# Kernel optimization log

Measured on AMD Instinct MI355X. Metric: run time of the kernel, lower is better.

## Reference

```python
import jax, jax.numpy as jnp
import numpy as np

N, E = 50000, 800000
IN_DIM, HID, HEADS, OUT = 128, 16, 8, 64
SLOPE = 0.2  # DGL GATConv default negative_slope


def setup_inputs() -> dict:
    key = jax.random.key(0)
    ks = jax.random.split(key, 12)
    return {
        "features": jax.random.normal(ks[0], (N, IN_DIM), jnp.float32),
        "src": jax.random.randint(ks[1], (E,), 0, N, jnp.int32),
        "dst": jax.random.randint(ks[2], (E,), 0, N, jnp.int32),
        "w": jax.random.uniform(ks[3], (E,), jnp.float32),
        "W1": jax.random.normal(ks[4], (IN_DIM, HEADS * HID), jnp.float32) / np.sqrt(IN_DIM),
        "al1": jax.random.normal(ks[5], (HEADS, HID), jnp.float32) * 0.1,
        "ar1": jax.random.normal(ks[6], (HEADS, HID), jnp.float32) * 0.1,
        "b1": jnp.zeros((HEADS * HID,), jnp.float32),
        "W2": jax.random.normal(ks[7], (HEADS * HID, OUT), jnp.float32) / np.sqrt(HEADS * HID),
        "al2": jax.random.normal(ks[8], (1, OUT), jnp.float32) * 0.1,
        "ar2": jax.random.normal(ks[9], (1, OUT), jnp.float32) * 0.1,
        "b2": jnp.zeros((OUT,), jnp.float32),
    }


def _gat_layer(x, src, dst, w, W, al, ar, b, heads, dout, act):
    """DGL GATConv with edge_weight: proj -> edge attn -> edge softmax(dst) -> * w -> scatter-sum."""
    n = x.shape[0]
    h = (x @ W).reshape(n, heads, dout)                 # [N,H,D]
    el = (h * al[None]).sum(-1)                         # [N,H] left attn logits
    er = (h * ar[None]).sum(-1)                         # [N,H] right attn logits
    e = el[src] + er[dst]                               # [E,H]
    e = jnp.where(e > 0, e, SLOPE * e)                  # leaky_relu
    m = jax.ops.segment_max(e, dst, num_segments=n)     # per-dst max for stable softmax
    a = jnp.exp(e - m[dst])
    z = jax.ops.segment_sum(a, dst, num_segments=n)
    a = (a / z[dst]) * w[:, None]                       # edge softmax scaled by edge weight
    msg = a[:, :, None] * h[src]                        # [E,H,D] gathered weighted messages
    rst = jax.ops.segment_sum(msg, dst, num_segments=n) # [N,H,D] scatter aggregation
    rst = rst + b.reshape(1, heads, dout)               # GATConv bias
    return act(rst) if act is not None else rst


def reference(features, src, dst, w, W1, al1, ar1, b1, W2, al2, ar2, b2):
    h = _gat_layer(features, src, dst, w, W1, al1, ar1, b1, HEADS, HID, jax.nn.relu)
    h = jax.nn.relu(h).reshape(N, HEADS * HID)          # outer F.relu + flatten(1)
    out = _gat_layer(h, src, dst, w, W2, al2, ar2, b2, 1, OUT, None)
    return out.squeeze(1)                               # [N,OUT]
```

## Files before the change

kernel.cpp:

```cpp
#include <hip/hip_runtime.h>
#include <hip/hip_fp16.h>

#define NN 50000
#define NE 800000

#define NBK 196
#define BSH 8
#define BMASK 255
#define SCAP 5120
#define CHUNK 1024
#define NBLK_A ((NE + CHUNK - 1) / CHUNK)

typedef _Float16 f16x8 __attribute__((ext_vector_type(8)));
typedef float f32x4 __attribute__((ext_vector_type(4)));


__global__ __launch_bounds__(256) void initg_k(int* gcur) {
    if (threadIdx.x < NBK) gcur[threadIdx.x] = 0;
}

__global__ __launch_bounds__(256) void sortA_k(const int* __restrict__ src,
                                               const int* __restrict__ dst,
                                               const float* __restrict__ wE,
                                               int* __restrict__ gcur,
                                               int2* __restrict__ stage) {
    __shared__ int hcnt[NBK], lexcl[NBK], lcur[NBK], gbase[NBK];
    __shared__ int wsum[4];
    __shared__ int2 lbuf[CHUNK];
    const int t = threadIdx.x;
    const int e0 = blockIdx.x * CHUNK;
    const int ne = min(CHUNK, NE - e0);
    if (t < NBK) { hcnt[t] = 0; lcur[t] = 0; }
    __syncthreads();
    for (int i = t; i < ne; i += 256) atomicAdd(&hcnt[dst[e0 + i] >> BSH], 1);
    __syncthreads();
    {
        const int lane = t & 63, wid = t >> 6;
        const int v = (t < NBK) ? hcnt[t] : 0;
        int s = v;
        #pragma unroll
        for (int off = 1; off < 64; off <<= 1) {
            int u = __shfl_up(s, off, 64);
            if (lane >= off) s += u;
        }
        if (lane == 63) wsum[wid] = s;
        __syncthreads();
        int add = 0;
        for (int w = 0; w < wid; w++) add += wsum[w];
        if (t < NBK) lexcl[t] = s - v + add;
    }
    __syncthreads();
    if (t < NBK && hcnt[t] > 0) gbase[t] = atomicAdd(&gcur[t], hcnt[t]);
    __syncthreads();
    for (int i = t; i < ne; i += 256) {
        const int d = dst[e0 + i];
        const int b = d >> BSH;
        const int r = atomicAdd(&lcur[b], 1);
        lbuf[lexcl[b] + r] = make_int2((src[e0 + i] & 0xFFFF) | ((d & BMASK) << 16),
                                       __float_as_int(wE[e0 + i]));
    }
    __syncthreads();
    const int wv = t >> 6, lane = t & 63;
    for (int b = wv; b < NBK; b += 4) {
        const int cnt = hcnt[b];
        if (cnt == 0) continue;
        const int lo = lexcl[b];
        int2* dp = stage + (size_t)b * SCAP + gbase[b];
        for (int j = lane; j < cnt; j += 64) dp[j] = lbuf[lo + j];
    }
}

__global__ __launch_bounds__(256) void scang_k(const int* __restrict__ gcur,
                                               int* __restrict__ gb2,
                                               int* __restrict__ offs_last) {
    __shared__ int wsum[4];
    const int t = threadIdx.x, lane = t & 63, wid = t >> 6;
    const int v = (t < NBK) ? gcur[t] : 0;
    int s = v;
    #pragma unroll
    for (int off = 1; off < 64; off <<= 1) {
        int u = __shfl_up(s, off, 64);
        if (lane >= off) s += u;
    }
    if (lane == 63) wsum[wid] = s;
    __syncthreads();
    int add = 0;
    for (int w = 0; w < wid; w++) add += wsum[w];
    if (t < NBK) gb2[t] = s - v + add;
    if (t == 0) offs_last[0] = NE;
}

__global__ __launch_bounds__(512) void sortB_k(const int* __restrict__ gcur,
                                               const int* __restrict__ gb2,
                                               const int2* __restrict__ stage,
                                               int* __restrict__ offs,
                                               unsigned int* __restrict__ csr) {
    __shared__ int cnt[256], cur[256];
    __shared__ int wsum[8];
    const int b = blockIdx.x, t = threadIdx.x;
    const int nb = gcur[b];
    const int base = gb2[b];
    const int dlo = b << BSH;
    if (t < 256) cnt[t] = 0;
    __syncthreads();
    const int2* sp = stage + (size_t)b * SCAP;
    for (int i = t; i < nb; i += 512) atomicAdd(&cnt[(sp[i].x >> 16) & BMASK], 1);
    __syncthreads();
    {
        const int lane = t & 63, wid = t >> 6;
        const int v = (t < 256) ? cnt[t] : 0;
        int s = v;
        #pragma unroll
        for (int off = 1; off < 64; off <<= 1) {
            int u = __shfl_up(s, off, 64);
            if (lane >= off) s += u;
        }
        if (lane == 63) wsum[wid] = s;
        __syncthreads();
        int add = 0;
        for (int w = 0; w < wid; w++) add += wsum[w];
        const int excl = s - v + add;
        if (t < 256) {
            cur[t] = excl;
            if (dlo + t < NN) offs[dlo + t] = base + excl;
        }
        if (t == 0) offs[min(dlo + 256, NN)] = base + nb;
    }
    __syncthreads();
    for (int i = t; i < nb; i += 512) {
        const int2 pr = sp[i];
        const int dloc = (pr.x >> 16) & BMASK;
        const int sv = pr.x & 0xFFFF;
        const int r = atomicAdd(&cur[dloc], 1);
        const __half hw = __float2half(__int_as_float(pr.y));
        csr[base + r] = (unsigned int)sv | ((unsigned int)__half_as_ushort(hw) << 16);
    }
}

__global__ __launch_bounds__(256) void convw_k(const float* __restrict__ W1,
                                               const float* __restrict__ W2,
                                               __half* __restrict__ w1t,
                                               __half* __restrict__ w2t) {
    int i = blockIdx.x * 256 + threadIdx.x;
    if (i < 128 * 128) {
        const int k = i >> 7, n = i & 127;
        w1t[(size_t)n * 128 + k] = __float2half(W1[i]);
    }
    if (i < 128 * 64) {
        const int k = i >> 6, n = i & 63;
        w2t[(size_t)n * 128 + k] = __float2half(W2[i]);
    }
}

__global__ __launch_bounds__(256) void proj1_k(const float* __restrict__ x,
                                               const __half* __restrict__ w1t,
                                               const float* __restrict__ al1,
                                               const float* __restrict__ ar1,
                                               __half* __restrict__ h1h,
                                               float* __restrict__ el1,
                                               float* __restrict__ er1) {
    const int t = threadIdx.x, l = t & 63, wv = t >> 6;
    const int rbase = blockIdx.x * 64 + wv * 16;
    const int cl = l & 15, kg = l >> 4;
    const int arow = rbase + cl;
    const float* xrow = x + (size_t)(arow < NN ? arow : NN - 1) * 128;
    f16x8 afrag[4];
    #pragma unroll
    for (int ks = 0; ks < 4; ks++) {
        const float4 u0 = *(const float4*)(xrow + ks * 32 + kg * 8);
        const float4 u1 = *(const float4*)(xrow + ks * 32 + kg * 8 + 4);
        f16x8 a;
        a[0] = (_Float16)u0.x; a[1] = (_Float16)u0.y; a[2] = (_Float16)u0.z; a[3] = (_Float16)u0.w;
        a[4] = (_Float16)u1.x; a[5] = (_Float16)u1.y; a[6] = (_Float16)u1.z; a[7] = (_Float16)u1.w;
        afrag[ks] = a;
    }
    f32x4 acc[8];
    #pragma unroll
    for (int nt = 0; nt < 8; nt++) { acc[nt][0]=0.f; acc[nt][1]=0.f; acc[nt][2]=0.f; acc[nt][3]=0.f; }
    #pragma unroll
    for (int nt = 0; nt < 8; nt++) {
        const f16x8* bp = (const f16x8*)(w1t + (size_t)(nt * 16 + cl) * 128 + kg * 8);
        #pragma unroll
        for (int ks = 0; ks < 4; ks++)
            acc[nt] = __builtin_amdgcn_mfma_f32_16x16x32_f16(afrag[ks], bp[ks * 4], acc[nt], 0, 0, 0);
    }
    const int orow0 = rbase + kg * 4;
    #pragma unroll
    for (int nt = 0; nt < 8; nt++) {
        const int col = nt * 16 + cl;
        const float alc = al1[col], arc = ar1[col];
        #pragma unroll
        for (int r = 0; r < 4; r++) {
            const float v = acc[nt][r];
            const int orow = orow0 + r;
            const bool ok = (orow < NN);
            if (ok) h1h[(size_t)orow * 128 + col] = __float2half(v);
            float pe = v * alc, pr = v * arc;
            #pragma unroll
            for (int m = 1; m < 16; m <<= 1) {
                pe += __shfl_xor(pe, m, 64);
                pr += __shfl_xor(pr, m, 64);
            }
            if (ok && cl == 0) {
                el1[(size_t)orow * 8 + nt] = pe;
                er1[(size_t)orow * 8 + nt] = pr;
            }
        }
    }
}

__global__ __launch_bounds__(128) void agg1_k(const int* __restrict__ offs,
                                              const unsigned int* __restrict__ csr,
                                              const __half* __restrict__ h1h,
                                              const float* __restrict__ el1,
                                              const float* __restrict__ er1,
                                              const float* __restrict__ b1,
                                              __half* __restrict__ h2in_h) {
    const int t = threadIdx.x, w = t >> 6, l = t & 63;
    const int n = blockIdx.x * 2 + w;
    const int beg = offs[n], deg = offs[n + 1] - beg;
    const int h = l & 7, g = l & 15, es = l >> 4, hg = g >> 1;
    const int e0 = l >> 3, e1 = e0 + 8;
    const float er_h = er1[(size_t)n * 8 + h];
    float z_lane = 0.f;
    float acc[8];
    #pragma unroll
    for (int j = 0; j < 8; j++) acc[j] = 0.f;
    const float4* hp4 = (const float4*)h1h;

    for (int base = 0; base < deg; base += 16) {
        int pr = 0;
        if (l < 16 && base + l < deg) pr = (int)csr[beg + base + l];
        const unsigned int pr0 = (unsigned int)__shfl(pr, e0, 64);
        const unsigned int pr1 = (unsigned int)__shfl(pr, e1, 64);
        float lg0 = -1e30f, lg1 = -1e30f;
        if (base + e0 < deg) {
            const float v = el1[(size_t)(pr0 & 0xFFFF) * 8 + h] + er_h;
            lg0 = v > 0.f ? v : 0.2f * v;
        }
        if (base + e1 < deg) {
            const float v = el1[(size_t)(pr1 & 0xFFFF) * 8 + h] + er_h;
            lg1 = v > 0.f ? v : 0.2f * v;
        }
        const float p0 = __expf(lg0);
        const float p1 = __expf(lg1);
        z_lane += p0 + p1;
        const float w0 = __half2float(__ushort_as_half((unsigned short)(pr0 >> 16)));
        const float w1 = __half2float(__ushort_as_half((unsigned short)(pr1 >> 16)));
        const float pw0 = p0 * w0, pw1 = p1 * w1;
        const int sA = __shfl(pr, es, 64) & 0xFFFF, sB = __shfl(pr, es + 4, 64) & 0xFFFF;
        const int sC = __shfl(pr, es + 8, 64) & 0xFFFF, sD = __shfl(pr, es + 12, 64) & 0xFFFF;
        const float pA = __shfl(pw0, es * 8 + hg, 64), pB = __shfl(pw0, (es + 4) * 8 + hg, 64);
        const float pC = __shfl(pw1, es * 8 + hg, 64), pD = __shfl(pw1, (es + 4) * 8 + hg, 64);
        const float4 vA = hp4[(size_t)sA * 16 + g];
        const float4 vB = hp4[(size_t)sB * 16 + g];
        const float4 vC = hp4[(size_t)sC * 16 + g];
        const float4 vD = hp4[(size_t)sD * 16 + g];
        #pragma unroll
        for (int q = 0; q < 4; q++) {
            const float2 fA = __half22float2(((const __half2*)&vA)[q]);
            const float2 fB = __half22float2(((const __half2*)&vB)[q]);
            const float2 fC = __half22float2(((const __half2*)&vC)[q]);
            const float2 fD = __half22float2(((const __half2*)&vD)[q]);
            acc[2 * q]     = fmaf(pA, fA.x, fmaf(pB, fB.x, fmaf(pC, fC.x, fmaf(pD, fD.x, acc[2 * q]))));
            acc[2 * q + 1] = fmaf(pA, fA.y, fmaf(pB, fB.y, fmaf(pC, fC.y, fmaf(pD, fD.y, acc[2 * q + 1]))));
        }
    }
    z_lane += __shfl_xor(z_lane, 8, 64);
    z_lane += __shfl_xor(z_lane, 16, 64);
    z_lane += __shfl_xor(z_lane, 32, 64);
    #pragma unroll
    for (int j = 0; j < 8; j++) {
        acc[j] += __shfl_xor(acc[j], 16, 64);
        acc[j] += __shfl_xor(acc[j], 32, 64);
    }
    const float zg = __shfl(z_lane, hg, 64);
    if (l < 16) {
        const float inv = (deg > 0) ? 1.f / zg : 0.f;
        const float4* b4 = (const float4*)b1;
        const float4 bb0 = b4[g * 2], bb1 = b4[g * 2 + 1];
        __half hv[8];
        hv[0] = __float2half(fmaxf(acc[0] * inv + bb0.x, 0.f));
        hv[1] = __float2half(fmaxf(acc[1] * inv + bb0.y, 0.f));
        hv[2] = __float2half(fmaxf(acc[2] * inv + bb0.z, 0.f));
        hv[3] = __float2half(fmaxf(acc[3] * inv + bb0.w, 0.f));
        hv[4] = __float2half(fmaxf(acc[4] * inv + bb1.x, 0.f));
        hv[5] = __float2half(fmaxf(acc[5] * inv + bb1.y, 0.f));
        hv[6] = __float2half(fmaxf(acc[6] * inv + bb1.z, 0.f));
        hv[7] = __float2half(fmaxf(acc[7] * inv + bb1.w, 0.f));
        *(int4*)(h2in_h + (size_t)n * 128 + g * 8) = *(const int4*)hv;
    }
}

__global__ __launch_bounds__(256) void proj2_k(const __half* __restrict__ xh,
                                               const __half* __restrict__ w2t,
                                               const float* __restrict__ al2,
                                               const float* __restrict__ ar2,
                                               __half* __restrict__ h2h,
                                               float* __restrict__ el2,
                                               float* __restrict__ er2) {
    const int t = threadIdx.x, l = t & 63, wv = t >> 6;
    const int rbase = blockIdx.x * 64 + wv * 16;
    const int cl = l & 15, kg = l >> 4;
    const int arow = rbase + cl;
    const __half* xrow = xh + (size_t)(arow < NN ? arow : NN - 1) * 128;
    f16x8 afrag[4];
    #pragma unroll
    for (int ks = 0; ks < 4; ks++)
        afrag[ks] = *(const f16x8*)(xrow + ks * 32 + kg * 8);
    f32x4 acc[4];
    #pragma unroll
    for (int nt = 0; nt < 4; nt++) { acc[nt][0]=0.f; acc[nt][1]=0.f; acc[nt][2]=0.f; acc[nt][3]=0.f; }
    #pragma unroll
    for (int nt = 0; nt < 4; nt++) {
        const f16x8* bp = (const f16x8*)(w2t + (size_t)(nt * 16 + cl) * 128 + kg * 8);
        #pragma unroll
        for (int ks = 0; ks < 4; ks++)
            acc[nt] = __builtin_amdgcn_mfma_f32_16x16x32_f16(afrag[ks], bp[ks * 4], acc[nt], 0, 0, 0);
    }
    const int orow0 = rbase + kg * 4;
    float pe[4] = {0.f, 0.f, 0.f, 0.f}, pr[4] = {0.f, 0.f, 0.f, 0.f};
    #pragma unroll
    for (int nt = 0; nt < 4; nt++) {
        const int col = nt * 16 + cl;
        const float alc = al2[col], arc = ar2[col];
        #pragma unroll
        for (int r = 0; r < 4; r++) {
            const float v = acc[nt][r];
            const int orow = orow0 + r;
            if (orow < NN) h2h[(size_t)orow * 64 + col] = __float2half(v);
            pe[r] = fmaf(v, alc, pe[r]);
            pr[r] = fmaf(v, arc, pr[r]);
        }
    }
    #pragma unroll
    for (int r = 0; r < 4; r++) {
        #pragma unroll
        for (int m = 1; m < 16; m <<= 1) {
            pe[r] += __shfl_xor(pe[r], m, 64);
            pr[r] += __shfl_xor(pr[r], m, 64);
        }
        const int orow = orow0 + r;
        if (cl == 0 && orow < NN) { el2[orow] = pe[r]; er2[orow] = pr[r]; }
    }
}

__global__ __launch_bounds__(128) void agg2_k(const int* __restrict__ offs,
                                              const unsigned int* __restrict__ csr,
                                              const __half* __restrict__ h2h,
                                              const float* __restrict__ el2,
                                              const float* __restrict__ er2,
                                              const float* __restrict__ b2,
                                              float* __restrict__ out) {
    const int t = threadIdx.x, w = t >> 6, l = t & 63;
    const int n = blockIdx.x * 2 + w;
    const int beg = offs[n], deg = offs[n + 1] - beg;
    const int g = l & 7, es = l >> 3;
    const int e = l & 15;
    const float erd = er2[n];
    float z_lane = 0.f;
    float acc[8];
    #pragma unroll
    for (int j = 0; j < 8; j++) acc[j] = 0.f;
    const float4* hp4 = (const float4*)h2h;

    for (int base = 0; base < deg; base += 16) {
        int pr = 0;
        if (l < 16 && base + l < deg) pr = (int)csr[beg + base + l];
        const unsigned int prE = (unsigned int)__shfl(pr, e, 64);
        float lg = -1e30f;
        if (base + e < deg) {
            const float v = el2[prE & 0xFFFF] + erd;
            lg = v > 0.f ? v : 0.2f * v;
        }
        const float p = __expf(lg);
        z_lane += p;
        const float pw = p * __half2float(__ushort_as_half((unsigned short)(prE >> 16)));
        const int sA = __shfl(pr, es, 64) & 0xFFFF, sB = __shfl(pr, es + 8, 64) & 0xFFFF;
        const float pA = __shfl(pw, es, 64), pB = __shfl(pw, es + 8, 64);
        const float4 vA = hp4[(size_t)sA * 8 + g];
        const float4 vB = hp4[(size_t)sB * 8 + g];
        #pragma unroll
        for (int q = 0; q < 4; q++) {
            const float2 fA = __half22float2(((const __half2*)&vA)[q]);
            const float2 fB = __half22float2(((const __half2*)&vB)[q]);
            acc[2 * q]     = fmaf(pA, fA.x, fmaf(pB, fB.x, acc[2 * q]));
            acc[2 * q + 1] = fmaf(pA, fA.y, fmaf(pB, fB.y, acc[2 * q + 1]));
        }
    }
    z_lane += __shfl_xor(z_lane, 1, 64);
    z_lane += __shfl_xor(z_lane, 2, 64);
    z_lane += __shfl_xor(z_lane, 4, 64);
    z_lane += __shfl_xor(z_lane, 8, 64);
    #pragma unroll
    for (int j = 0; j < 8; j++) {
        acc[j] += __shfl_xor(acc[j], 8, 64);
        acc[j] += __shfl_xor(acc[j], 16, 64);
        acc[j] += __shfl_xor(acc[j], 32, 64);
    }
    if (l < 8) {
        const float inv = (deg > 0) ? 1.f / z_lane : 0.f;
        const float4* b4 = (const float4*)b2;
        const float4 bb0 = b4[g * 2], bb1 = b4[g * 2 + 1];
        float4 o0, o1;
        o0.x = acc[0] * inv + bb0.x;
        o0.y = acc[1] * inv + bb0.y;
        o0.z = acc[2] * inv + bb0.z;
        o0.w = acc[3] * inv + bb0.w;
        o1.x = acc[4] * inv + bb1.x;
        o1.y = acc[5] * inv + bb1.y;
        o1.z = acc[6] * inv + bb1.z;
        o1.w = acc[7] * inv + bb1.w;
        float4* op = (float4*)(out + (size_t)n * 64 + g * 8);
        op[0] = o0; op[1] = o1;
    }
}


extern "C" void kernel_launch(void* const* d_in, const int* in_sizes, int n_in,
                              void* d_out, int out_size, void* d_ws, size_t ws_size,
                              hipStream_t stream) {
    const float* feat = (const float*)d_in[0];
    const int*   srcv = (const int*)d_in[1];
    const int*   dstv = (const int*)d_in[2];
    const float* wE   = (const float*)d_in[3];
    const float* W1   = (const float*)d_in[4];
    const float* al1  = (const float*)d_in[5];
    const float* ar1  = (const float*)d_in[6];
    const float* b1   = (const float*)d_in[7];
    const float* W2   = (const float*)d_in[8];
    const float* al2  = (const float*)d_in[9];
    const float* ar2  = (const float*)d_in[10];
    const float* b2   = (const float*)d_in[11];
    float* out = (float*)d_out;

    char* ws = (char*)d_ws;
    size_t off = 0;
    auto take = [&](size_t bytes) -> char* {
        char* pp = ws + off;
        off = (off + bytes + 255) & ~(size_t)255;
        return pp;
    };
    __half* h1h   = (__half*)take((size_t)NN * 128 * 2);
    __half* h2h   = (__half*)take((size_t)NN * 64 * 2);
    __half* h2in_h= (__half*)take((size_t)NN * 128 * 2);
    float* el1  = (float*)take((size_t)NN * 8 * 4);
    float* er1  = (float*)take((size_t)NN * 8 * 4);
    float* el2  = (float*)take((size_t)NN * 4);
    float* er2  = (float*)take((size_t)NN * 4);
    int* offs   = (int*)take((size_t)(NN + 1) * 4);
    unsigned int* csr = (unsigned int*)take((size_t)NE * 4);
    int* gcur   = (int*)take((size_t)NBK * 4);
    int* gb2    = (int*)take((size_t)NBK * 4);
    __half* w1t = (__half*)take((size_t)128 * 128 * 2);
    __half* w2t = (__half*)take((size_t)64 * 128 * 2);
    int2* stage = (int2*)h2in_h;

    initg_k<<<1, 256, 0, stream>>>(gcur);
    sortA_k<<<NBLK_A, 256, 0, stream>>>(srcv, dstv, wE, gcur, stage);
    scang_k<<<1, 256, 0, stream>>>(gcur, gb2, offs + NN);
    sortB_k<<<NBK, 512, 0, stream>>>(gcur, gb2, stage, offs, csr);
    convw_k<<<64, 256, 0, stream>>>(W1, W2, w1t, w2t);
    proj1_k<<<(NN + 63) / 64, 256, 0, stream>>>(feat, w1t, al1, ar1, h1h, el1, er1);
    agg1_k<<<NN / 2, 128, 0, stream>>>(offs, csr, h1h, el1, er1, b1, h2in_h);
    proj2_k<<<(NN + 63) / 64, 256, 0, stream>>>(h2in_h, w2t, al2, ar2, h2h, el2, er2);
    agg2_k<<<NN / 2, 128, 0, stream>>>(offs, csr, h2h, el2, er2, b2, out);
}
```

Measured before the change: 160.9 us.

## Fuse sort/projection launches and widen edge batches in aggregation kernels

Merges weight conversion with counter init, runs the edge bucketing and layer-1 projection as one horizontally fused launch, and folds the bucket-offset scan into sortB, which now uses 1024 threads. This cuts the pipeline from nine launches to six and drops the separate scan pass. Both aggregation kernels now take 32 edges per iteration and prefetch the next CSR chunk, so more gathers are in flight per wave. The costs are higher register pressure in the aggregation loops and each sortB block redoing a small prefix sum.

After: 152.6 us. 5.2% less time.

```diff
diff --git a/kernel.cpp b/kernel.cpp
--- a/kernel.cpp
+++ b/kernel.cpp
@@ -10,102 +10,162 @@
 #define SCAP 5120
 #define CHUNK 1024
 #define NBLK_A ((NE + CHUNK - 1) / CHUNK)
+#define NBLK_P ((NN + 63) / 64)
 
 typedef _Float16 f16x8 __attribute__((ext_vector_type(8)));
 typedef float f32x4 __attribute__((ext_vector_type(4)));
 
-
-__global__ __launch_bounds__(256) void initg_k(int* gcur) {
-    if (threadIdx.x < NBK) gcur[threadIdx.x] = 0;
-}
-
-__global__ __launch_bounds__(256) void sortA_k(const int* __restrict__ src,
-                                               const int* __restrict__ dst,
-                                               const float* __restrict__ wE,
-                                               int* __restrict__ gcur,
-                                               int2* __restrict__ stage) {
-    __shared__ int hcnt[NBK], lexcl[NBK], lcur[NBK], gbase[NBK];
+__global__ __launch_bounds__(256) void init_k(const float* __restrict__ W1,
+                                              const float* __restrict__ W2,
+                                              __half* __restrict__ w1t,
+                                              __half* __restrict__ w2t,
+                                              int* __restrict__ gcur) {
+    const int i = blockIdx.x * 256 + threadIdx.x;
+    {
+        const int k = i >> 7, n = i & 127;
+        w1t[n * 128 + k] = __float2half(W1[i]);
+    }
+    if (i < 128 * 64) {
+        const int k = i >> 6, n = i & 63;
+        w2t[n * 128 + k] = __float2half(W2[i]);
+    }
+    if (i < NBK) gcur[i] = 0;
+}
+
+__global__ __launch_bounds__(256) void sortA_proj1_k(const int* __restrict__ src,
+                                                     const int* __restrict__ dst,
+                                                     const float* __restrict__ wE,
+                                                     int* __restrict__ gcur,
+                                                     int2* __restrict__ stage,
+                                                     const float* __restrict__ x,
+                                                     const __half* __restrict__ w1t,
+                                                     const float* __restrict__ al1,
+                                                     const float* __restrict__ ar1,
+                                                     __half* __restrict__ h1h,
+                                                     float* __restrict__ el1,
+                                                     float* __restrict__ er1) {
+    const int t = threadIdx.x;
+    if (blockIdx.x < NBLK_A) {
+        __shared__ int hcnt[NBK], lexcl[NBK], lcur[NBK], gbase[NBK];
+        __shared__ int wsum[4];
+        __shared__ int2 lbuf[CHUNK];
+        const int e0 = blockIdx.x * CHUNK;
+        const int ne = min(CHUNK, NE - e0);
+        if (t < NBK) { hcnt[t] = 0; lcur[t] = 0; }
+        __syncthreads();
+        for (int i = t; i < ne; i += 256) atomicAdd(&hcnt[dst[e0 + i] >> BSH], 1);
+        __syncthreads();
+        {
+            const int lane = t & 63, wid = t >> 6;
+            const int v = (t < NBK) ? hcnt[t] : 0;
+            int s = v;
+            #pragma unroll
+            for (int off = 1; off < 64; off <<= 1) {
+                int u = __shfl_up(s, off, 64);
+                if (lane >= off) s += u;
+            }
+            if (lane == 63) wsum[wid] = s;
+            __syncthreads();
+            int add = 0;
+            for (int w = 0; w < wid; w++) add += wsum[w];
+            if (t < NBK) lexcl[t] = s - v + add;
+        }
+        __syncthreads();
+        if (t < NBK && hcnt[t] > 0) gbase[t] = atomicAdd(&gcur[t], hcnt[t]);
+        __syncthreads();
+        for (int i = t; i < ne; i += 256) {
+            const int d = dst[e0 + i];
+            const int b = d >> BSH;
+            const int r = atomicAdd(&lcur[b], 1);
+            lbuf[lexcl[b] + r] = make_int2((src[e0 + i] & 0xFFFF) | ((d & BMASK) << 16),
+                                           __float_as_int(wE[e0 + i]));
+        }
+        __syncthreads();
+        const int wv = t >> 6, lane = t & 63;
+        for (int b = wv; b < NBK; b += 4) {
+            const int cnt = hcnt[b];
+            if (cnt == 0) continue;
+            const int lo = lexcl[b];
+            int2* dp = stage + (size_t)b * SCAP + gbase[b];
+            for (int j = lane; j < cnt; j += 64) dp[j] = lbuf[lo + j];
+        }
+    } else {
+        const int bid = blockIdx.x - NBLK_A;
+        const int l = t & 63, wv = t >> 6;
+        const int rbase = bid * 64 + wv * 16;
+        const int cl = l & 15, kg = l >> 4;
+        const int arow = rbase + cl;
+        const float* xrow = x + (size_t)(arow < NN ? arow : NN - 1) * 128;
+        f16x8 afrag[4];
+        #pragma unroll
+        for (int ks = 0; ks < 4; ks++) {
+            const float4 u0 = *(const float4*)(xrow + ks * 32 + kg * 8);
+            const float4 u1 = *(const float4*)(xrow + ks * 32 + kg * 8 + 4);
+            f16x8 a;
+            a[0] = (_Float16)u0.x; a[1] = (_Float16)u0.y; a[2] = (_Float16)u0.z; a[3] = (_Float16)u0.w;
+            a[4] = (_Float16)u1.x; a[5] = (_Float16)u1.y; a[6] = (_Float16)u1.z; a[7] = (_Float16)u1.w;
+            afrag[ks] = a;
+        }
+        f32x4 acc[8];
+        #pragma unroll
+        for (int nt = 0; nt < 8; nt++) { acc[nt][0]=0.f; acc[nt][1]=0.f; acc[nt][2]=0.f; acc[nt][3]=0.f; }
+        #pragma unroll
+        for (int nt = 0; nt < 8; nt++) {
+            const f16x8* bp = (const f16x8*)(w1t + (size_t)(nt * 16 + cl) * 128 + kg * 8);
+            #pragma unroll
+            for (int ks = 0; ks < 4; ks++)
+                acc[nt] = __builtin_amdgcn_mfma_f32_16x16x32_f16(afrag[ks], bp[ks * 4], acc[nt], 0, 0, 0);
+        }
+        const int orow0 = rbase + kg * 4;
+        #pragma unroll
+        for (int nt = 0; nt < 8; nt++) {
+            const int col = nt * 16 + cl;
+            const float alc = al1[col], arc = ar1[col];
+            #pragma unroll
+            for (int r = 0; r < 4; r++) {
+                const float v = acc[nt][r];
+                const int orow = orow0 + r;
+                const bool ok = (orow < NN);
+                if (ok) h1h[(size_t)orow * 128 + col] = __float2half(v);
+                float pe = v * alc, pr = v * arc;
+                #pragma unroll
+                for (int m = 1; m < 16; m <<= 1) {
+                    pe += __shfl_xor(pe, m, 64);
+                    pr += __shfl_xor(pr, m, 64);
+                }
+                if (ok && cl == 0) {
+                    el1[(size_t)orow * 8 + nt] = pe;
+                    er1[(size_t)orow * 8 + nt] = pr;
+                }
+            }
+        }
+    }
+}
+
+__global__ __launch_bounds__(1024) void sortB_k(const int* __restrict__ gcur,
+                                                const int2* __restrict__ stage,
+                                                int* __restrict__ offs,
+                                                unsigned int* __restrict__ csr) {
+    __shared__ int cnt[256], cur[256], gall[NBK];
     __shared__ int wsum[4];
-    __shared__ int2 lbuf[CHUNK];
-    const int t = threadIdx.x;
-    const int e0 = blockIdx.x * CHUNK;
-    const int ne = min(CHUNK, NE - e0);
-    if (t < NBK) { hcnt[t] = 0; lcur[t] = 0; }
-    __syncthreads();
-    for (int i = t; i < ne; i += 256) atomicAdd(&hcnt[dst[e0 + i] >> BSH], 1);
-    __syncthreads();
-    {
-        const int lane = t & 63, wid = t >> 6;
-        const int v = (t < NBK) ? hcnt[t] : 0;
-        int s = v;
-        #pragma unroll
-        for (int off = 1; off < 64; off <<= 1) {
-            int u = __shfl_up(s, off, 64);
-            if (lane >= off) s += u;
-        }
-        if (lane == 63) wsum[wid] = s;
-        __syncthreads();
-        int add = 0;
-        for (int w = 0; w < wid; w++) add += wsum[w];
-        if (t < NBK) lexcl[t] = s - v + add;
-    }
-    __syncthreads();
-    if (t < NBK && hcnt[t] > 0) gbase[t] = atomicAdd(&gcur[t], hcnt[t]);
-    __syncthreads();
-    for (int i = t; i < ne; i += 256) {
-        const int d = dst[e0 + i];
-        const int b = d >> BSH;
-        const int r = atomicAdd(&lcur[b], 1);
-        lbuf[lexcl[b] + r] = make_int2((src[e0 + i] & 0xFFFF) | ((d & BMASK) << 16),
-                                       __float_as_int(wE[e0 + i]));
-    }
-    __syncthreads();
-    const int wv = t >> 6, lane = t & 63;
-    for (int b = wv; b < NBK; b += 4) {
-        const int cnt = hcnt[b];
-        if (cnt == 0) continue;
-        const int lo = lexcl[b];
-        int2* dp = stage + (size_t)b * SCAP + gbase[b];
-        for (int j = lane; j < cnt; j += 64) dp[j] = lbuf[lo + j];
-    }
-}
-
-__global__ __launch_bounds__(256) void scang_k(const int* __restrict__ gcur,
-                                               int* __restrict__ gb2,
-                                               int* __restrict__ offs_last) {
-    __shared__ int wsum[4];
-    const int t = threadIdx.x, lane = t & 63, wid = t >> 6;
-    const int v = (t < NBK) ? gcur[t] : 0;
-    int s = v;
-    #pragma unroll
-    for (int off = 1; off < 64; off <<= 1) {
-        int u = __shfl_up(s, off, 64);
-        if (lane >= off) s += u;
-    }
-    if (lane == 63) wsum[wid] = s;
-    __syncthreads();
-    int add = 0;
-    for (int w = 0; w < wid; w++) add += wsum[w];
-    if (t < NBK) gb2[t] = s - v + add;
-    if (t == 0) offs_last[0] = NE;
-}
-
-__global__ __launch_bounds__(512) void sortB_k(const int* __restrict__ gcur,
-                                               const int* __restrict__ gb2,
-                                               const int2* __restrict__ stage,
-                                               int* __restrict__ offs,
-                                               unsigned int* __restrict__ csr) {
-    __shared__ int cnt[256], cur[256];
-    __shared__ int wsum[8];
+    __shared__ int sbase;
     const int b = blockIdx.x, t = threadIdx.x;
-    const int nb = gcur[b];
-    const int base = gb2[b];
-    const int dlo = b << BSH;
+    if (t < NBK) gall[t] = gcur[t];
     if (t < 256) cnt[t] = 0;
     __syncthreads();
+    const int nb = gall[b];
+    if (t < 64) {
+        int part = 0;
+        for (int i = t; i < b; i += 64) part += gall[i];
+        #pragma unroll
+        for (int m = 1; m < 64; m <<= 1) part += __shfl_xor(part, m, 64);
+        if (t == 0) sbase = part;
+    }
     const int2* sp = stage + (size_t)b * SCAP;
-    for (int i = t; i < nb; i += 512) atomicAdd(&cnt[(sp[i].x >> 16) & BMASK], 1);
+    for (int i = t; i < nb; i += 1024) atomicAdd(&cnt[(sp[i].x >> 16) & BMASK], 1);
     __syncthreads();
+    const int base = sbase;
+    const int dlo = b << BSH;
     {
         const int lane = t & 63, wid = t >> 6;
         const int v = (t < 256) ? cnt[t] : 0;
@@ -115,97 +175,25 @@
             int u = __shfl_up(s, off, 64);
             if (lane >= off) s += u;
         }
-        if (lane == 63) wsum[wid] = s;
-        __syncthreads();
-        int add = 0;
-        for (int w = 0; w < wid; w++) add += wsum[w];
-        const int excl = s - v + add;
+        if (t < 256 && lane == 63) wsum[wid] = s;
+        __syncthreads();
         if (t < 256) {
+            int add = 0;
+            for (int w = 0; w < wid; w++) add += wsum[w];
+            const int excl = s - v + add;
             cur[t] = excl;
             if (dlo + t < NN) offs[dlo + t] = base + excl;
         }
-        if (t == 0) offs[min(dlo + 256, NN)] = base + nb;
+        if (b == NBK - 1 && t == 0) offs[NN] = base + nb;
     }
     __syncthreads();
-    for (int i = t; i < nb; i += 512) {
+    for (int i = t; i < nb; i += 1024) {
         const int2 pr = sp[i];
         const int dloc = (pr.x >> 16) & BMASK;
         const int sv = pr.x & 0xFFFF;
         const int r = atomicAdd(&cur[dloc], 1);
         const __half hw = __float2half(__int_as_float(pr.y));
         csr[base + r] = (unsigned int)sv | ((unsigned int)__half_as_ushort(hw) << 16);
-    }
-}
-
-__global__ __launch_bounds__(256) void convw_k(const float* __restrict__ W1,
-                                               const float* __restrict__ W2,
-                                               __half* __restrict__ w1t,
-                                               __half* __restrict__ w2t) {
-    int i = blockIdx.x * 256 + threadIdx.x;
-    if (i < 128 * 128) {
-        const int k = i >> 7, n = i & 127;
-        w1t[(size_t)n * 128 + k] = __float2half(W1[i]);
-    }
-    if (i < 128 * 64) {
-        const int k = i >> 6, n = i & 63;
-        w2t[(size_t)n * 128 + k] = __float2half(W2[i]);
-    }
-}
-
-__global__ __launch_bounds__(256) void proj1_k(const float* __restrict__ x,
-                                               const __half* __restrict__ w1t,
-                                               const float* __restrict__ al1,
-                                               const float* __restrict__ ar1,
-                                               __half* __restrict__ h1h,
-                                               float* __restrict__ el1,
-                                               float* __restrict__ er1) {
-    const int t = threadIdx.x, l = t & 63, wv = t >> 6;
-    const int rbase = blockIdx.x * 64 + wv * 16;
-    const int cl = l & 15, kg = l >> 4;
-    const int arow = rbase + cl;
-    const float* xrow = x + (size_t)(arow < NN ? arow : NN - 1) * 128;
-    f16x8 afrag[4];
-    #pragma unroll
-    for (int ks = 0; ks < 4; ks++) {
-        const float4 u0 = *(const float4*)(xrow + ks * 32 + kg * 8);
-        const float4 u1 = *(const float4*)(xrow + ks * 32 + kg * 8 + 4);
-        f16x8 a;
-        a[0] = (_Float16)u0.x; a[1] = (_Float16)u0.y; a[2] = (_Float16)u0.z; a[3] = (_Float16)u0.w;
-        a[4] = (_Float16)u1.x; a[5] = (_Float16)u1.y; a[6] = (_Float16)u1.z; a[7] = (_Float16)u1.w;
-        afrag[ks] = a;
-    }
-    f32x4 acc[8];
-    #pragma unroll
-    for (int nt = 0; nt < 8; nt++) { acc[nt][0]=0.f; acc[nt][1]=0.f; acc[nt][2]=0.f; acc[nt][3]=0.f; }
-    #pragma unroll
-    for (int nt = 0; nt < 8; nt++) {
-        const f16x8* bp = (const f16x8*)(w1t + (size_t)(nt * 16 + cl) * 128 + kg * 8);
-        #pragma unroll
-        for (int ks = 0; ks < 4; ks++)
-            acc[nt] = __builtin_amdgcn_mfma_f32_16x16x32_f16(afrag[ks], bp[ks * 4], acc[nt], 0, 0, 0);
-    }
-    const int orow0 = rbase + kg * 4;
-    #pragma unroll
-    for (int nt = 0; nt < 8; nt++) {
-        const int col = nt * 16 + cl;
-        const float alc = al1[col], arc = ar1[col];
-        #pragma unroll
-        for (int r = 0; r < 4; r++) {
-            const float v = acc[nt][r];
-            const int orow = orow0 + r;
-            const bool ok = (orow < NN);
-            if (ok) h1h[(size_t)orow * 128 + col] = __float2half(v);
-            float pe = v * alc, pr = v * arc;
-            #pragma unroll
-            for (int m = 1; m < 16; m <<= 1) {
-                pe += __shfl_xor(pe, m, 64);
-                pr += __shfl_xor(pr, m, 64);
-            }
-            if (ok && cl == 0) {
-                el1[(size_t)orow * 8 + nt] = pe;
-                er1[(size_t)orow * 8 + nt] = pr;
-            }
-        }
     }
 }
 
@@ -219,8 +207,8 @@
     const int t = threadIdx.x, w = t >> 6, l = t & 63;
     const int n = blockIdx.x * 2 + w;
     const int beg = offs[n], deg = offs[n + 1] - beg;
-    const int h = l & 7, g = l & 15, es = l >> 4, hg = g >> 1;
-    const int e0 = l >> 3, e1 = e0 + 8;
+    const int h = l & 7, eb = l >> 3;
+    const int g = l & 15, es = l >> 4, hg = g >> 1;
     const float er_h = er1[(size_t)n * 8 + h];
     float z_lane = 0.f;
     float acc[8];
@@ -228,43 +216,47 @@
     for (int j = 0; j < 8; j++) acc[j] = 0.f;
     const float4* hp4 = (const float4*)h1h;
 
-    for (int base = 0; base < deg; base += 16) {
-        int pr = 0;
-        if (l < 16 && base + l < deg) pr = (int)csr[beg + base + l];
-        const unsigned int pr0 = (unsigned int)__shfl(pr, e0, 64);
-        const unsigned int pr1 = (unsigned int)__shfl(pr, e1, 64);
-        float lg0 = -1e30f, lg1 = -1e30f;
-        if (base + e0 < deg) {
-            const float v = el1[(size_t)(pr0 & 0xFFFF) * 8 + h] + er_h;
-            lg0 = v > 0.f ? v : 0.2f * v;
-        }
-        if (base + e1 < deg) {
-            const float v = el1[(size_t)(pr1 & 0xFFFF) * 8 + h] + er_h;
-            lg1 = v > 0.f ? v : 0.2f * v;
-        }
-        const float p0 = __expf(lg0);
-        const float p1 = __expf(lg1);
-        z_lane += p0 + p1;
-        const float w0 = __half2float(__ushort_as_half((unsigned short)(pr0 >> 16)));
-        const float w1 = __half2float(__ushort_as_half((unsigned short)(pr1 >> 16)));
-        const float pw0 = p0 * w0, pw1 = p1 * w1;
-        const int sA = __shfl(pr, es, 64) & 0xFFFF, sB = __shfl(pr, es + 4, 64) & 0xFFFF;
-        const int sC = __shfl(pr, es + 8, 64) & 0xFFFF, sD = __shfl(pr, es + 12, 64) & 0xFFFF;
-        const float pA = __shfl(pw0, es * 8 + hg, 64), pB = __shfl(pw0, (es + 4) * 8 + hg, 64);
-        const float pC = __shfl(pw1, es * 8 + hg, 64), pD = __shfl(pw1, (es + 4) * 8 + hg, 64);
-        const float4 vA = hp4[(size_t)sA * 16 + g];
-        const float4 vB = hp4[(size_t)sB * 16 + g];
-        const float4 vC = hp4[(size_t)sC * 16 + g];
-        const float4 vD = hp4[(size_t)sD * 16 + g];
-        #pragma unroll
-        for (int q = 0; q < 4; q++) {
-            const float2 fA = __half22float2(((const __half2*)&vA)[q]);
-            const float2 fB = __half22float2(((const __half2*)&vB)[q]);
-            const float2 fC = __half22float2(((const __half2*)&vC)[q]);
-            const float2 fD = __half22float2(((const __half2*)&vD)[q]);
-            acc[2 * q]     = fmaf(pA, fA.x, fmaf(pB, fB.x, fmaf(pC, fC.x, fmaf(pD, fD.x, acc[2 * q]))));
-            acc[2 * q + 1] = fmaf(pA, fA.y, fmaf(pB, fB.y, fmaf(pC, fC.y, fmaf(pD, fD.y, acc[2 * q + 1]))));
-        }
+    int pr = 0;
+    if (l < 32 && l < deg) pr = (int)csr[beg + l];
+    for (int base = 0; base < deg; base += 32) {
+        int prn = 0;
+        const int nbase = base + 32;
+        if (nbase < deg && l < 32 && nbase + l < deg) prn = (int)csr[beg + nbase + l];
+        float pwv[4];
+        #pragma unroll
+        for (int k = 0; k < 4; k++) {
+            const unsigned int pre = (unsigned int)__shfl(pr, eb + 8 * k, 64);
+            float lg = -1e30f;
+            if (base + eb + 8 * k < deg) {
+                const float v = el1[(size_t)(pre & 0xFFFF) * 8 + h] + er_h;
+                lg = v > 0.f ? v : 0.2f * v;
+            }
+            const float p = __expf(lg);
+            z_lane += p;
+            pwv[k] = p * __half2float(__ushort_as_half((unsigned short)(pre >> 16)));
+        }
+        int sv[8];
+        float pp[8];
+        #pragma unroll
+        for (int k = 0; k < 8; k++) sv[k] = __shfl(pr, es + 4 * k, 64) & 0xFFFF;
+        #pragma unroll
+        for (int k = 0; k < 8; k++) {
+            const int slane = ((es + 4 * (k & 1)) << 3) | hg;
+            pp[k] = __shfl(pwv[k >> 1], slane, 64);
+        }
+        float4 vv[8];
+        #pragma unroll
+        for (int k = 0; k < 8; k++) vv[k] = hp4[(size_t)sv[k] * 16 + g];
+        #pragma unroll
+        for (int k = 0; k < 8; k++) {
+            #pragma unroll
+            for (int q = 0; q < 4; q++) {
+                const float2 f = __half22float2(((const __half2*)&vv[k])[q]);
+                acc[2 * q]     = fmaf(pp[k], f.x, acc[2 * q]);
+                acc[2 * q + 1] = fmaf(pp[k], f.y, acc[2 * q + 1]);
+            }
+        }
+        pr = prn;
     }
     z_lane += __shfl_xor(z_lane, 8, 64);
     z_lane += __shfl_xor(z_lane, 16, 64);
@@ -356,7 +348,6 @@
     const int n = blockIdx.x * 2 + w;
     const int beg = offs[n], deg = offs[n + 1] - beg;
     const int g = l & 7, es = l >> 3;
-    const int e = l & 15;
     const float erd = er2[n];
     float z_lane = 0.f;
     float acc[8];
@@ -364,34 +355,47 @@
     for (int j = 0; j < 8; j++) acc[j] = 0.f;
     const float4* hp4 = (const float4*)h2h;
 
-    for (int base = 0; base < deg; base += 16) {
-        int pr = 0;
-        if (l < 16 && base + l < deg) pr = (int)csr[beg + base + l];
-        const unsigned int prE = (unsigned int)__shfl(pr, e, 64);
-        float lg = -1e30f;
-        if (base + e < deg) {
-            const float v = el2[prE & 0xFFFF] + erd;
-            lg = v > 0.f ? v : 0.2f * v;
-        }
-        const float p = __expf(lg);
-        z_lane += p;
-        const float pw = p * __half2float(__ushort_as_half((unsigned short)(prE >> 16)));
-        const int sA = __shfl(pr, es, 64) & 0xFFFF, sB = __shfl(pr, es + 8, 64) & 0xFFFF;
-        const float pA = __shfl(pw, es, 64), pB = __shfl(pw, es + 8, 64);
-        const float4 vA = hp4[(size_t)sA * 8 + g];
-        const float4 vB = hp4[(size_t)sB * 8 + g];
-        #pragma unroll
-        for (int q = 0; q < 4; q++) {
-            const float2 fA = __half22float2(((const __half2*)&vA)[q]);
-            const float2 fB = __half22float2(((const __half2*)&vB)[q]);
-            acc[2 * q]     = fmaf(pA, fA.x, fmaf(pB, fB.x, acc[2 * q]));
-            acc[2 * q + 1] = fmaf(pA, fA.y, fmaf(pB, fB.y, acc[2 * q + 1]));
-        }
+    int pr = 0;
+    if (l < 32 && l < deg) pr = (int)csr[beg + l];
+    for (int base = 0; base < deg; base += 32) {
+        int prn = 0;
+        const int nbase = base + 32;
+        if (nbase < deg && l < 32 && nbase + l < deg) prn = (int)csr[beg + nbase + l];
+        float pw = 0.f;
+        if (l < 32 && base + l < deg) {
+            const float v = el2[(unsigned int)pr & 0xFFFF] + erd;
+            const float lg = v > 0.f ? v : 0.2f * v;
+            const float p = __expf(lg);
+            z_lane += p;
+            pw = p * __half2float(__ushort_as_half((unsigned short)((unsigned int)pr >> 16)));
+        }
+        int sv[4];
+        float pp[4];
+        #pragma unroll
+        for (int k = 0; k < 4; k++) {
+            sv[k] = __shfl(pr, es + 8 * k, 64) & 0xFFFF;
+            pp[k] = __shfl(pw, es + 8 * k, 64);
+        }
+        float4 vv[4];
+        #pragma unroll
+        for (int k = 0; k < 4; k++) vv[k] = hp4[(size_t)sv[k] * 8 + g];
+        #pragma unroll
+        for (int k = 0; k < 4; k++) {
+            #pragma unroll
+            for (int q = 0; q < 4; q++) {
+                const float2 f = __half22float2(((const __half2*)&vv[k])[q]);
+                acc[2 * q]     = fmaf(pp[k], f.x, acc[2 * q]);
+                acc[2 * q + 1] = fmaf(pp[k], f.y, acc[2 * q + 1]);
+            }
+        }
+        pr = prn;
     }
     z_lane += __shfl_xor(z_lane, 1, 64);
     z_lane += __shfl_xor(z_lane, 2, 64);
     z_lane += __shfl_xor(z_lane, 4, 64);
     z_lane += __shfl_xor(z_lane, 8, 64);
+    z_lane += __shfl_xor(z_lane, 16, 64);
+    z_lane += __shfl_xor(z_lane, 32, 64);
     #pragma unroll
     for (int j = 0; j < 8; j++) {
         acc[j] += __shfl_xor(acc[j], 8, 64);
@@ -451,17 +455,14 @@
     int* offs   = (int*)take((size_t)(NN + 1) * 4);
     unsigned int* csr = (unsigned int*)take((size_t)NE * 4);
     int* gcur   = (int*)take((size_t)NBK * 4);
-    int* gb2    = (int*)take((size_t)NBK * 4);
     __half* w1t = (__half*)take((size_t)128 * 128 * 2);
     __half* w2t = (__half*)take((size_t)64 * 128 * 2);
     int2* stage = (int2*)h2in_h;
 
-    initg_k<<<1, 256, 0, stream>>>(gcur);
-    sortA_k<<<NBLK_A, 256, 0, stream>>>(srcv, dstv, wE, gcur, stage);
-    scang_k<<<1, 256, 0, stream>>>(gcur, gb2, offs + NN);
-    sortB_k<<<NBK, 512, 0, stream>>>(gcur, gb2, stage, offs, csr);
-    convw_k<<<64, 256, 0, stream>>>(W1, W2, w1t, w2t);
-    proj1_k<<<(NN + 63) / 64, 256, 0, stream>>>(feat, w1t, al1, ar1, h1h, el1, er1);
+    init_k<<<64, 256, 0, stream>>>(W1, W2, w1t, w2t, gcur);
+    sortA_proj1_k<<<NBLK_A + NBLK_P, 256, 0, stream>>>(srcv, dstv, wE, gcur, stage,
+                                                       feat, w1t, al1, ar1, h1h, el1, er1);
+    sortB_k<<<NBK, 1024, 0, stream>>>(gcur, stage, offs, csr);
     agg1_k<<<NN / 2, 128, 0, stream>>>(offs, csr, h1h, el1, er1, b1, h2in_h);
     proj2_k<<<(NN + 63) / 64, 256, 0, stream>>>(h2in_h, w2t, al2, ar2, h2h, el2, er2);
     agg2_k<<<NN / 2, 128, 0, stream>>>(offs, csr, h2h, el2, er2, b2, out);
```
